# Kernel optimization log

Measured on AMD Instinct MI355X. Metric: run time of the kernel, lower is better.

The kernel has to match this reference:

```python
import jax, jax.numpy as jnp
import numpy as np

H = 128          # hidden_size
L = 3            # num_layers
N = 200_000      # total atoms across all fragments
E = 400_000      # bidirectional bonds (avg degree ~2)
G = 8192         # number of molecular subgraphs
ATOM_V = 120
BOND_V = 5


def setup_inputs() -> dict:
    key = jax.random.key(0)
    ks = jax.random.split(key, 14)
    s = 1.0 / np.sqrt(H)
    f = lambda k, shp: (jax.random.normal(k, shp, jnp.float32) * s)
    return {
        "atom_types": jax.random.randint(ks[0], (N,), 0, ATOM_V),
        "edges": jax.random.randint(ks[1], (2, E), 0, N),
        "edge_types": jax.random.randint(ks[2], (E,), 0, BOND_V),
        "node_batch": jnp.sort(jax.random.randint(ks[3], (N,), 0, G)),
        "atom_emb": f(ks[4], (ATOM_V, H)),
        "bond_emb": f(ks[5], (BOND_V, H)),
        "conv_w1": f(ks[6], (L, H, H)),
        "conv_b1": jnp.zeros((L, H), jnp.float32),
        "conv_w2": f(ks[7], (L, H, H)),
        "conv_b2": jnp.zeros((L, H), jnp.float32),
        "proj_w1": f(ks[8], (H, H)),
        "proj_b1": jnp.zeros((H,), jnp.float32),
        "proj_w2": f(ks[9], (H, H)),
        "proj_b2": jnp.zeros((H,), jnp.float32),
    }


def reference(atom_types, edges, edge_types, node_batch,
              atom_emb, bond_emb,
              conv_w1, conv_b1, conv_w2, conv_b2,
              proj_w1, proj_b1, proj_w2, proj_b2):
    # node / bond embeddings (torch clamps indices to vocab-1)
    x = atom_emb[jnp.clip(atom_types, 0, ATOM_V - 1)]       # [N, H]
    a = bond_emb[jnp.clip(edge_types, 0, BOND_V - 1)]       # [E, H]
    src, dst = edges[0], edges[1]
    # GINEConv layers: x_i' = MLP(x_i + sum_{j->i} ReLU(x_j + e_ji)), eps=0
    for l in range(L):
        m = jax.nn.relu(x[src] + a)                         # [E, H] edge messages
        agg = jax.ops.segment_sum(m, dst, num_segments=N)   # scatter-add to dst nodes
        h = x + agg
        h = jax.nn.relu(h @ conv_w1[l] + conv_b1[l])
        x = h @ conv_w2[l] + conv_b2[l]
    # per-graph mean readout
    sums = jax.ops.segment_sum(x, node_batch, num_segments=G)                      # [G, H]
    cnt = jax.ops.segment_sum(jnp.ones((N, 1), x.dtype), node_batch, num_segments=G)
    g = sums / jnp.maximum(cnt, 1.0)
    # proj: Linear -> SiLU -> Linear
    g = jax.nn.silu(g @ proj_w1 + proj_b1)
    return g @ proj_w2 + proj_b2                            # [G, H]
```

## Files before the change

kernel.cpp:

```cpp
#include <hip/hip_runtime.h>

typedef unsigned short u16;
typedef __attribute__((ext_vector_type(8))) short short8;
typedef __attribute__((ext_vector_type(4))) float f32x4;

#define HDIM 128
#define SCAN_B 512

__device__ __forceinline__ float bf2f(u16 v) {
    return __uint_as_float(((unsigned int)v) << 16);
}
__device__ __forceinline__ u16 f2bf(float f) {
    unsigned int u = __float_as_uint(f);
    unsigned int r = (u + 0x7FFFu + ((u >> 16) & 1u)) >> 16;
    return (u16)r;
}

__global__ __launch_bounds__(256) void prep_kernel(
    const float* __restrict__ w1, const float* __restrict__ w2,
    const float* __restrict__ pw1, const float* __restrict__ pw2,
    const float* __restrict__ atom_emb,
    u16* __restrict__ wt, u16* __restrict__ ebf)
{
    int gid = blockIdx.x * 256 + threadIdx.x;
    if (gid < 8 * 16384) {
        int mat = gid >> 14;
        int idx = gid & 16383;
        int n = idx >> 7, k = idx & 127;
        const float* src;
        if      (mat < 3) src = w1 + mat * 16384;
        else if (mat < 6) src = w2 + (mat - 3) * 16384;
        else if (mat == 6) src = pw1;
        else               src = pw2;
        wt[gid] = f2bf(src[k * 128 + n]);
    } else {
        int i = gid - 8 * 16384;
        if (i < 120 * 128) ebf[i] = f2bf(atom_emb[i]);
    }
}

__global__ __launch_bounds__(256) void deg_hist_kernel(
    const int* __restrict__ edges, int* __restrict__ deg, int E, int N)
{
    int e = blockIdx.x * 256 + threadIdx.x;
    if (e >= E) return;
    int d = edges[E + e];
    d = d < 0 ? 0 : (d >= N ? N - 1 : d);
    atomicAdd(&deg[d], 1);
}

__global__ __launch_bounds__(SCAN_B) void scan_block_kernel(
    const int* __restrict__ deg, int* __restrict__ offs, int* __restrict__ bsum, int N)
{
    __shared__ int tmp[SCAN_B];
    int t = threadIdx.x;
    int gid = blockIdx.x * SCAN_B + t;
    int v = (gid < N) ? deg[gid] : 0;
    tmp[t] = v;
    __syncthreads();
#pragma unroll
    for (int off = 1; off < SCAN_B; off <<= 1) {
        int add = (t >= off) ? tmp[t - off] : 0;
        __syncthreads();
        tmp[t] += add;
        __syncthreads();
    }
    if (gid < N) offs[gid] = tmp[t] - v;
    if (t == SCAN_B - 1) bsum[blockIdx.x] = tmp[t];
}

__global__ __launch_bounds__(1024) void scan_partials_kernel(int* __restrict__ bsum, int nblk)
{
    __shared__ int tmp[1024];
    int t = threadIdx.x;
    int v = (t < nblk) ? bsum[t] : 0;
    tmp[t] = v;
    __syncthreads();
#pragma unroll
    for (int off = 1; off < 1024; off <<= 1) {
        int add = (t >= off) ? tmp[t - off] : 0;
        __syncthreads();
        tmp[t] += add;
        __syncthreads();
    }
    if (t < nblk) bsum[t] = tmp[t] - v;
}

__global__ __launch_bounds__(256) void finalize_offs_kernel(
    int* __restrict__ offs, const int* __restrict__ bsum,
    int* __restrict__ cursor, int N, int E)
{
    int gid = blockIdx.x * 256 + threadIdx.x;
    if (gid < N) {
        int v = offs[gid] + bsum[gid / SCAN_B];
        offs[gid] = v;
        cursor[gid] = v;
    }
    if (gid == 0) offs[N] = E;
}

__global__ __launch_bounds__(256) void fill_csr_kernel(
    const int* __restrict__ edges, const int* __restrict__ etypes,
    int* __restrict__ cursor, int* __restrict__ csr, int E, int N)
{
    int e = blockIdx.x * 256 + threadIdx.x;
    if (e >= E) return;
    int s = edges[e], d = edges[E + e], t = etypes[e];
    s = s < 0 ? 0 : (s >= N ? N - 1 : s);
    d = d < 0 ? 0 : (d >= N ? N - 1 : d);
    t = t < 0 ? 0 : (t > 4 ? 4 : t);
    int pos = atomicAdd(&cursor[d], 1);
    csr[pos] = (s << 3) | t;
}

__global__ __launch_bounds__(512, 4) void gine_kernel(
    const u16* __restrict__ x_in, u16* __restrict__ x_out,
    const int* __restrict__ types, int use_emb, const u16* __restrict__ ebf,
    const int* __restrict__ offs, const int* __restrict__ csr,
    const float* __restrict__ bond_emb,
    const u16* __restrict__ w1t, const float* __restrict__ b1,
    const u16* __restrict__ w2t, const float* __restrict__ b2, int N)
{
    __shared__ __align__(16) u16 As[128][136];
    __shared__ __align__(16) u16 Ws[128][136];
    __shared__ __align__(16) u16 bsh[5 * 128];
    const int tid  = threadIdx.x;
    const int row0 = blockIdx.x * 128;
    const int wave = tid >> 6, lane = tid & 63;
    const int m = lane & 15, quad = lane >> 4;

    for (int i = tid; i < 640; i += 512) bsh[i] = f2bf(bond_emb[i]);
    {
        const uint4* src = (const uint4*)w1t;
        for (int i = tid; i < 2048; i += 512) {
            int n = i >> 4, k8 = i & 15;
            *(uint4*)&Ws[n][k8 * 8] = src[i];
        }
    }
    {
        const int rp = tid >> 4, c8 = (tid & 15) * 8;
        __syncthreads();
        for (int pass = 0; pass < 2; pass++) {
            int rA = (pass * 2 + 0) * 32 + rp;
            int rB = (pass * 2 + 1) * 32 + rp;
            int rowA = row0 + rA, rowB = row0 + rB;
            int rcA = rowA < N ? rowA : N - 1;
            int rcB = rowB < N ? rowB : N - 1;
            const u16 *spA, *spB;
            if (use_emb) {
                int tA = types[rcA]; tA = tA < 0 ? 0 : (tA > 119 ? 119 : tA);
                int tB = types[rcB]; tB = tB < 0 ? 0 : (tB > 119 ? 119 : tB);
                spA = ebf + (size_t)tA * 128;
                spB = ebf + (size_t)tB * 128;
            } else {
                spA = x_in + (size_t)rcA * 128;
                spB = x_in + (size_t)rcB * 128;
            }
            int jbA = offs[rcA], jeA = rowA < N ? offs[rcA + 1] : jbA;
            int jbB = offs[rcB], jeB = rowB < N ? offs[rcB + 1] : jbB;
            uint4 svA = *(const uint4*)(spA + c8);
            uint4 svB = *(const uint4*)(spB + c8);
            float accA[8], accB[8];
            {
                const u16* pA = (const u16*)&svA;
                const u16* pB = (const u16*)&svB;
#pragma unroll
                for (int i = 0; i < 8; i++) { accA[i] = bf2f(pA[i]); accB[i] = bf2f(pB[i]); }
            }
            int dA = jeA - jbA, dB = jeB - jbB;
            int dmax = dA > dB ? dA : dB;
            for (int k = 0; k < dmax; k += 2) {
                bool a0 = (k    ) < dA;
                bool a1 = (k + 1) < dA;
                bool a2 = (k    ) < dB;
                bool a3 = (k + 1) < dB;
                int v0 = a0 ? csr[jbA + k]     : 0;
                int v1 = a1 ? csr[jbA + k + 1] : 0;
                int v2 = a2 ? csr[jbB + k]     : 0;
                int v3 = a3 ? csr[jbB + k + 1] : 0;
                const u16 *g0p, *g1p, *g2p, *g3p;
                if (use_emb) {
                    int t0 = types[v0 >> 3]; t0 = t0 < 0 ? 0 : (t0 > 119 ? 119 : t0);
                    int t1 = types[v1 >> 3]; t1 = t1 < 0 ? 0 : (t1 > 119 ? 119 : t1);
                    int t2 = types[v2 >> 3]; t2 = t2 < 0 ? 0 : (t2 > 119 ? 119 : t2);
                    int t3 = types[v3 >> 3]; t3 = t3 < 0 ? 0 : (t3 > 119 ? 119 : t3);
                    g0p = ebf + (size_t)t0 * 128; g1p = ebf + (size_t)t1 * 128;
                    g2p = ebf + (size_t)t2 * 128; g3p = ebf + (size_t)t3 * 128;
                } else {
                    g0p = x_in + (size_t)(v0 >> 3) * 128;
                    g1p = x_in + (size_t)(v1 >> 3) * 128;
                    g2p = x_in + (size_t)(v2 >> 3) * 128;
                    g3p = x_in + (size_t)(v3 >> 3) * 128;
                }
                uint4 g0 = *(const uint4*)(g0p + c8);
                uint4 g1 = *(const uint4*)(g1p + c8);
                uint4 g2 = *(const uint4*)(g2p + c8);
                uint4 g3 = *(const uint4*)(g3p + c8);
                if (a0) {
                    const u16* gp = (const u16*)&g0; const u16* bp = bsh + (v0 & 7) * 128 + c8;
#pragma unroll
                    for (int i = 0; i < 8; i++) { float mm = bf2f(gp[i]) + bf2f(bp[i]); accA[i] += mm > 0.f ? mm : 0.f; }
                }
                if (a1) {
                    const u16* gp = (const u16*)&g1; const u16* bp = bsh + (v1 & 7) * 128 + c8;
#pragma unroll
                    for (int i = 0; i < 8; i++) { float mm = bf2f(gp[i]) + bf2f(bp[i]); accA[i] += mm > 0.f ? mm : 0.f; }
                }
                if (a2) {
                    const u16* gp = (const u16*)&g2; const u16* bp = bsh + (v2 & 7) * 128 + c8;
#pragma unroll
                    for (int i = 0; i < 8; i++) { float mm = bf2f(gp[i]) + bf2f(bp[i]); accB[i] += mm > 0.f ? mm : 0.f; }
                }
                if (a3) {
                    const u16* gp = (const u16*)&g3; const u16* bp = bsh + (v3 & 7) * 128 + c8;
#pragma unroll
                    for (int i = 0; i < 8; i++) { float mm = bf2f(gp[i]) + bf2f(bp[i]); accB[i] += mm > 0.f ? mm : 0.f; }
                }
            }
            uint4 ovA = make_uint4(0u, 0u, 0u, 0u), ovB = make_uint4(0u, 0u, 0u, 0u);
            if (rowA < N) {
                u16* op = (u16*)&ovA;
#pragma unroll
                for (int i = 0; i < 8; i++) op[i] = f2bf(accA[i]);
            }
            if (rowB < N) {
                u16* op = (u16*)&ovB;
#pragma unroll
                for (int i = 0; i < 8; i++) op[i] = f2bf(accB[i]);
            }
            *(uint4*)&As[rA][c8] = ovA;
            *(uint4*)&As[rB][c8] = ovB;
        }
    }
    __syncthreads();

    f32x4 acc[8];
#pragma unroll
    for (int c = 0; c < 8; c++) acc[c] = (f32x4){0.f, 0.f, 0.f, 0.f};
#pragma unroll
    for (int q = 0; q < 4; q++) {
        short8 a = *(const short8*)&As[wave * 16 + m][q * 32 + quad * 8];
#pragma unroll
        for (int c = 0; c < 8; c++) {
            short8 b = *(const short8*)&Ws[c * 16 + m][q * 32 + quad * 8];
            acc[c] = __builtin_amdgcn_mfma_f32_16x16x32_bf16(a, b, acc[c], 0, 0, 0);
        }
    }
    __syncthreads();
    {
        const uint4* src = (const uint4*)w2t;
        for (int i = tid; i < 2048; i += 512) {
            int n = i >> 4, k8 = i & 15;
            *(uint4*)&Ws[n][k8 * 8] = src[i];
        }
    }
#pragma unroll
    for (int c = 0; c < 8; c++) {
        int col = c * 16 + m;
        float bias = b1[col];
#pragma unroll
        for (int r = 0; r < 4; r++) {
            float v = acc[c][r] + bias;
            v = v > 0.f ? v : 0.f;
            As[wave * 16 + quad * 4 + r][col] = f2bf(v);
        }
    }
    __syncthreads();
    f32x4 acc2[8];
#pragma unroll
    for (int c = 0; c < 8; c++) acc2[c] = (f32x4){0.f, 0.f, 0.f, 0.f};
#pragma unroll
    for (int q = 0; q < 4; q++) {
        short8 a = *(const short8*)&As[wave * 16 + m][q * 32 + quad * 8];
#pragma unroll
        for (int c = 0; c < 8; c++) {
            short8 b = *(const short8*)&Ws[c * 16 + m][q * 32 + quad * 8];
            acc2[c] = __builtin_amdgcn_mfma_f32_16x16x32_bf16(a, b, acc2[c], 0, 0, 0);
        }
    }
    __syncthreads();
#pragma unroll
    for (int c = 0; c < 8; c++) {
        int col = c * 16 + m;
        float bias = b2[col];
#pragma unroll
        for (int r = 0; r < 4; r++)
            As[wave * 16 + quad * 4 + r][col] = f2bf(acc2[c][r] + bias);
    }
    __syncthreads();
    for (int i = tid; i < 2048; i += 512) {
        int r = i >> 4, c8 = (i & 15) * 8;
        int row = row0 + r;
        if (row < N) *(uint4*)(x_out + (size_t)row * 128 + c8) = *(const uint4*)&As[r][c8];
    }
}

__global__ __launch_bounds__(256) void readout_mean_kernel(
    const u16* __restrict__ x, const int* __restrict__ nb,
    u16* __restrict__ gm, int N)
{
    __shared__ int range[2];
    __shared__ float part[16][128];
    int b = blockIdx.x;
    int tid = threadIdx.x;
    if (tid < 2) {
        int target = b + tid;
        int lo = 0, hi = N;
        while (lo < hi) {
            int mid = (lo + hi) >> 1;
            if (nb[mid] < target) lo = mid + 1; else hi = mid;
        }
        range[tid] = lo;
    }
    __syncthreads();
    int s = range[0], e = range[1];
    int rg = tid >> 4, c8 = (tid & 15) * 8;
    float acc[8];
#pragma unroll
    for (int i = 0; i < 8; i++) acc[i] = 0.f;
    for (int n = s + rg; n < e; n += 16) {
        uint4 v = *(const uint4*)(x + (size_t)n * 128 + c8);
        const u16* vp = (const u16*)&v;
#pragma unroll
        for (int i = 0; i < 8; i++) acc[i] += bf2f(vp[i]);
    }
#pragma unroll
    for (int i = 0; i < 8; i++) part[rg][c8 + i] = acc[i];
    __syncthreads();
    if (tid < 128) {
        float sum = 0.f;
#pragma unroll
        for (int g = 0; g < 16; g++) sum += part[g][tid];
        float cnt = (float)((e - s) > 0 ? (e - s) : 1);
        gm[(size_t)b * 128 + tid] = f2bf(sum / cnt);
    }
}

__global__ __launch_bounds__(256) void proj_kernel(
    const u16* __restrict__ gm, float* __restrict__ out,
    const u16* __restrict__ pw1t, const float* __restrict__ pb1,
    const u16* __restrict__ pw2t, const float* __restrict__ pb2, int G)
{
    __shared__ __align__(16) u16 As[64][136];
    __shared__ __align__(16) u16 Ws[128][136];
    const int tid  = threadIdx.x;
    const int row0 = blockIdx.x * 64;
    const int wave = tid >> 6, lane = tid & 63;
    const int m = lane & 15, quad = lane >> 4;

    {
        const uint4* src = (const uint4*)pw1t;
        for (int i = tid; i < 2048; i += 256) {
            int n = i >> 4, k8 = i & 15;
            *(uint4*)&Ws[n][k8 * 8] = src[i];
        }
    }
    for (int i = tid; i < 1024; i += 256) {
        int r = i >> 4, c8 = (i & 15) * 8;
        int row = row0 + r;
        uint4 ov = make_uint4(0u, 0u, 0u, 0u);
        if (row < G) ov = *(const uint4*)(gm + (size_t)row * 128 + c8);
        *(uint4*)&As[r][c8] = ov;
    }
    __syncthreads();
    f32x4 acc[8];
#pragma unroll
    for (int c = 0; c < 8; c++) acc[c] = (f32x4){0.f, 0.f, 0.f, 0.f};
#pragma unroll
    for (int q = 0; q < 4; q++) {
        short8 a = *(const short8*)&As[wave * 16 + m][q * 32 + quad * 8];
#pragma unroll
        for (int c = 0; c < 8; c++) {
            short8 b = *(const short8*)&Ws[c * 16 + m][q * 32 + quad * 8];
            acc[c] = __builtin_amdgcn_mfma_f32_16x16x32_bf16(a, b, acc[c], 0, 0, 0);
        }
    }
    __syncthreads();
    {
        const uint4* src = (const uint4*)pw2t;
        for (int i = tid; i < 2048; i += 256) {
            int n = i >> 4, k8 = i & 15;
            *(uint4*)&Ws[n][k8 * 8] = src[i];
        }
    }
#pragma unroll
    for (int c = 0; c < 8; c++) {
        int col = c * 16 + m;
        float bias = pb1[col];
#pragma unroll
        for (int r = 0; r < 4; r++) {
            float v = acc[c][r] + bias;
            v = v / (1.f + __expf(-v));
            As[wave * 16 + quad * 4 + r][col] = f2bf(v);
        }
    }
    __syncthreads();
    f32x4 acc2[8];
#pragma unroll
    for (int c = 0; c < 8; c++) acc2[c] = (f32x4){0.f, 0.f, 0.f, 0.f};
#pragma unroll
    for (int q = 0; q < 4; q++) {
        short8 a = *(const short8*)&As[wave * 16 + m][q * 32 + quad * 8];
#pragma unroll
        for (int c = 0; c < 8; c++) {
            short8 b = *(const short8*)&Ws[c * 16 + m][q * 32 + quad * 8];
            acc2[c] = __builtin_amdgcn_mfma_f32_16x16x32_bf16(a, b, acc2[c], 0, 0, 0);
        }
    }
#pragma unroll
    for (int c = 0; c < 8; c++) {
        int col = c * 16 + m;
        float bias = pb2[col];
#pragma unroll
        for (int r = 0; r < 4; r++) {
            int row = row0 + quad * 4 + r + wave * 16;
            if (row < G) out[(size_t)row * 128 + col] = acc2[c][r] + bias;
        }
    }
}

extern "C" void kernel_launch(void* const* d_in, const int* in_sizes, int n_in,
                              void* d_out, int out_size, void* d_ws, size_t ws_size,
                              hipStream_t stream) {
    const int*   atom_types  = (const int*)d_in[0];
    const int*   edges       = (const int*)d_in[1];
    const int*   edge_types  = (const int*)d_in[2];
    const int*   node_batch  = (const int*)d_in[3];
    const float* atom_emb    = (const float*)d_in[4];
    const float* bond_emb    = (const float*)d_in[5];
    const float* conv_w1     = (const float*)d_in[6];
    const float* conv_b1     = (const float*)d_in[7];
    const float* conv_w2     = (const float*)d_in[8];
    const float* conv_b2     = (const float*)d_in[9];
    const float* pw1         = (const float*)d_in[10];
    const float* pb1         = (const float*)d_in[11];
    const float* pw2         = (const float*)d_in[12];
    const float* pb2         = (const float*)d_in[13];
    float* out = (float*)d_out;

    const int N = in_sizes[0];
    const int E = in_sizes[2];
    const int G = out_size / HDIM;
    const int nblk = (N + SCAN_B - 1) / SCAN_B;

    size_t xA_bytes  = (size_t)N * HDIM * sizeof(u16);
    size_t xB_bytes  = (size_t)N * HDIM * sizeof(u16);
    size_t wt_bytes  = (size_t)8 * HDIM * HDIM * sizeof(u16);
    size_t ebf_bytes = (size_t)120 * HDIM * sizeof(u16);
    size_t gm_bytes  = (size_t)G * HDIM * sizeof(u16);
    size_t deg_bytes = (size_t)N * 4;
    size_t off_bytes = (size_t)(N + 1) * 4;
    size_t cur_bytes = (size_t)N * 4;
    size_t bs_bytes  = 1024 * 4;
    size_t csr_bytes = (size_t)E * 4;
    size_t need = xA_bytes + xB_bytes + wt_bytes + ebf_bytes + gm_bytes +
                  deg_bytes + off_bytes + cur_bytes + bs_bytes + csr_bytes;
    if (ws_size < need) {
        hipMemsetAsync(d_out, 0, (size_t)out_size * sizeof(float), stream);
        return;
    }
    char* p = (char*)d_ws;
    u16* xA   = (u16*)p;  p += xA_bytes;
    u16* xB   = (u16*)p;  p += xB_bytes;
    u16* wt   = (u16*)p;  p += wt_bytes;
    u16* ebf  = (u16*)p;  p += ebf_bytes;
    u16* gm   = (u16*)p;  p += gm_bytes;
    int* deg  = (int*)p;  p += deg_bytes;
    int* offs = (int*)p;  p += off_bytes;
    int* cur  = (int*)p;  p += cur_bytes;
    int* bsum = (int*)p;  p += bs_bytes;
    int* csr  = (int*)p;

    prep_kernel<<<(8 * 16384 + 120 * 128 + 255) / 256, 256, 0, stream>>>(
        conv_w1, conv_w2, pw1, pw2, atom_emb, wt, ebf);

    hipMemsetAsync(deg, 0, deg_bytes, stream);
    deg_hist_kernel<<<(E + 255) / 256, 256, 0, stream>>>(edges, deg, E, N);
    scan_block_kernel<<<nblk, SCAN_B, 0, stream>>>(deg, offs, bsum, N);
    scan_partials_kernel<<<1, 1024, 0, stream>>>(bsum, nblk);
    finalize_offs_kernel<<<(N + 255) / 256, 256, 0, stream>>>(offs, bsum, cur, N, E);
    fill_csr_kernel<<<(E + 255) / 256, 256, 0, stream>>>(edges, edge_types, cur, csr, E, N);

    const int gblocks = (N + 127) / 128;
    gine_kernel<<<gblocks, 512, 0, stream>>>(
        xB , xA, atom_types, 1, ebf, offs, csr, bond_emb,
        wt + 0 * 16384, conv_b1 + 0, wt + 3 * 16384, conv_b2 + 0, N);
    gine_kernel<<<gblocks, 512, 0, stream>>>(
        xA, xB, atom_types, 0, ebf, offs, csr, bond_emb,
        wt + 1 * 16384, conv_b1 + 128, wt + 4 * 16384, conv_b2 + 128, N);
    gine_kernel<<<gblocks, 512, 0, stream>>>(
        xB, xA, atom_types, 0, ebf, offs, csr, bond_emb,
        wt + 2 * 16384, conv_b1 + 256, wt + 5 * 16384, conv_b2 + 256, N);

    readout_mean_kernel<<<G, 256, 0, stream>>>(xA, node_batch, gm, N);
    proj_kernel<<<(G + 63) / 64, 256, 0, stream>>>(
        gm, out, wt + 6 * 16384, pb1, wt + 7 * 16384, pb2, G);
}
```

Before: 371.4 us.

## Fuse readout into projection, drop partial scan kernel, gather four rows

Merges the per-graph mean readout into the projection kernel so pooled features stay in shared memory, and removes the separate block-partial scan by having each finalize block reduce its own prefix. The gine gather loop now handles four destination rows per thread at once to raise memory-level parallelism. The fused readout runs with far fewer blocks and walks 64 graphs serially with barriers per graph, which may reduce parallelism in that phase.

```diff
diff --git a/kernel.cpp b/kernel.cpp
--- a/kernel.cpp
+++ b/kernel.cpp
@@ -69,30 +69,26 @@
     if (t == SCAN_B - 1) bsum[blockIdx.x] = tmp[t];
 }
 
-__global__ __launch_bounds__(1024) void scan_partials_kernel(int* __restrict__ bsum, int nblk)
-{
-    __shared__ int tmp[1024];
-    int t = threadIdx.x;
-    int v = (t < nblk) ? bsum[t] : 0;
-    tmp[t] = v;
-    __syncthreads();
-#pragma unroll
-    for (int off = 1; off < 1024; off <<= 1) {
-        int add = (t >= off) ? tmp[t - off] : 0;
-        __syncthreads();
-        tmp[t] += add;
-        __syncthreads();
-    }
-    if (t < nblk) bsum[t] = tmp[t] - v;
-}
-
 __global__ __launch_bounds__(256) void finalize_offs_kernel(
     int* __restrict__ offs, const int* __restrict__ bsum,
     int* __restrict__ cursor, int N, int E)
 {
-    int gid = blockIdx.x * 256 + threadIdx.x;
+    __shared__ int red[256];
+    const int tid = threadIdx.x;
+    const int B = blockIdx.x >> 1;
+    int sum = 0;
+    for (int t = tid; t < B; t += 256) sum += bsum[t];
+    red[tid] = sum;
+    __syncthreads();
+#pragma unroll
+    for (int off = 128; off > 0; off >>= 1) {
+        if (tid < off) red[tid] += red[tid + off];
+        __syncthreads();
+    }
+    int prefix = red[0];
+    int gid = blockIdx.x * 256 + tid;
     if (gid < N) {
-        int v = offs[gid] + bsum[gid / SCAN_B];
+        int v = offs[gid] + prefix;
         offs[gid] = v;
         cursor[gid] = v;
     }
@@ -140,97 +136,126 @@
     {
         const int rp = tid >> 4, c8 = (tid & 15) * 8;
         __syncthreads();
-        for (int pass = 0; pass < 2; pass++) {
-            int rA = (pass * 2 + 0) * 32 + rp;
-            int rB = (pass * 2 + 1) * 32 + rp;
-            int rowA = row0 + rA, rowB = row0 + rB;
-            int rcA = rowA < N ? rowA : N - 1;
-            int rcB = rowB < N ? rowB : N - 1;
-            const u16 *spA, *spB;
+
+        int rowA = row0 + rp,      rowB = row0 + 32 + rp;
+        int rowC = row0 + 64 + rp, rowD = row0 + 96 + rp;
+        int rcA = rowA < N ? rowA : N - 1;
+        int rcB = rowB < N ? rowB : N - 1;
+        int rcC = rowC < N ? rowC : N - 1;
+        int rcD = rowD < N ? rowD : N - 1;
+        const u16 *spA, *spB, *spC, *spD;
+        if (use_emb) {
+            int tA = types[rcA]; tA = tA < 0 ? 0 : (tA > 119 ? 119 : tA);
+            int tB = types[rcB]; tB = tB < 0 ? 0 : (tB > 119 ? 119 : tB);
+            int tC = types[rcC]; tC = tC < 0 ? 0 : (tC > 119 ? 119 : tC);
+            int tD = types[rcD]; tD = tD < 0 ? 0 : (tD > 119 ? 119 : tD);
+            spA = ebf + (size_t)tA * 128; spB = ebf + (size_t)tB * 128;
+            spC = ebf + (size_t)tC * 128; spD = ebf + (size_t)tD * 128;
+        } else {
+            spA = x_in + (size_t)rcA * 128; spB = x_in + (size_t)rcB * 128;
+            spC = x_in + (size_t)rcC * 128; spD = x_in + (size_t)rcD * 128;
+        }
+        int jbA = offs[rcA], jeA = rowA < N ? offs[rcA + 1] : jbA;
+        int jbB = offs[rcB], jeB = rowB < N ? offs[rcB + 1] : jbB;
+        int jbC = offs[rcC], jeC = rowC < N ? offs[rcC + 1] : jbC;
+        int jbD = offs[rcD], jeD = rowD < N ? offs[rcD + 1] : jbD;
+        uint4 svA = *(const uint4*)(spA + c8);
+        uint4 svB = *(const uint4*)(spB + c8);
+        uint4 svC = *(const uint4*)(spC + c8);
+        uint4 svD = *(const uint4*)(spD + c8);
+        float accA[8], accB[8], accC[8], accD[8];
+        {
+            const u16* pA = (const u16*)&svA; const u16* pB = (const u16*)&svB;
+            const u16* pC = (const u16*)&svC; const u16* pD = (const u16*)&svD;
+#pragma unroll
+            for (int i = 0; i < 8; i++) {
+                accA[i] = bf2f(pA[i]); accB[i] = bf2f(pB[i]);
+                accC[i] = bf2f(pC[i]); accD[i] = bf2f(pD[i]);
+            }
+        }
+        int dA = jeA - jbA, dB = jeB - jbB, dC = jeC - jbC, dD = jeD - jbD;
+        int dmax = dA > dB ? dA : dB;
+        dmax = dC > dmax ? dC : dmax;
+        dmax = dD > dmax ? dD : dmax;
+        for (int k = 0; k < dmax; k += 2) {
+            bool a0 = k < dA,     a1 = (k + 1) < dA;
+            bool a2 = k < dB,     a3 = (k + 1) < dB;
+            bool a4 = k < dC,     a5 = (k + 1) < dC;
+            bool a6 = k < dD,     a7 = (k + 1) < dD;
+            int v0 = a0 ? csr[jbA + k] : 0;  int v1 = a1 ? csr[jbA + k + 1] : 0;
+            int v2 = a2 ? csr[jbB + k] : 0;  int v3 = a3 ? csr[jbB + k + 1] : 0;
+            int v4 = a4 ? csr[jbC + k] : 0;  int v5 = a5 ? csr[jbC + k + 1] : 0;
+            int v6 = a6 ? csr[jbD + k] : 0;  int v7 = a7 ? csr[jbD + k + 1] : 0;
+            const u16 *p0, *p1, *p2, *p3, *p4, *p5, *p6, *p7;
             if (use_emb) {
-                int tA = types[rcA]; tA = tA < 0 ? 0 : (tA > 119 ? 119 : tA);
-                int tB = types[rcB]; tB = tB < 0 ? 0 : (tB > 119 ? 119 : tB);
-                spA = ebf + (size_t)tA * 128;
-                spB = ebf + (size_t)tB * 128;
+                int t0 = types[v0 >> 3]; t0 = t0 < 0 ? 0 : (t0 > 119 ? 119 : t0);
+                int t1 = types[v1 >> 3]; t1 = t1 < 0 ? 0 : (t1 > 119 ? 119 : t1);
+                int t2 = types[v2 >> 3]; t2 = t2 < 0 ? 0 : (t2 > 119 ? 119 : t2);
+                int t3 = types[v3 >> 3]; t3 = t3 < 0 ? 0 : (t3 > 119 ? 119 : t3);
+                int t4 = types[v4 >> 3]; t4 = t4 < 0 ? 0 : (t4 > 119 ? 119 : t4);
+                int t5 = types[v5 >> 3]; t5 = t5 < 0 ? 0 : (t5 > 119 ? 119 : t5);
+                int t6 = types[v6 >> 3]; t6 = t6 < 0 ? 0 : (t6 > 119 ? 119 : t6);
+                int t7 = types[v7 >> 3]; t7 = t7 < 0 ? 0 : (t7 > 119 ? 119 : t7);
+                p0 = ebf + (size_t)t0 * 128; p1 = ebf + (size_t)t1 * 128;
+                p2 = ebf + (size_t)t2 * 128; p3 = ebf + (size_t)t3 * 128;
+                p4 = ebf + (size_t)t4 * 128; p5 = ebf + (size_t)t5 * 128;
+                p6 = ebf + (size_t)t6 * 128; p7 = ebf + (size_t)t7 * 128;
             } else {
-                spA = x_in + (size_t)rcA * 128;
-                spB = x_in + (size_t)rcB * 128;
+                p0 = x_in + (size_t)(v0 >> 3) * 128; p1 = x_in + (size_t)(v1 >> 3) * 128;
+                p2 = x_in + (size_t)(v2 >> 3) * 128; p3 = x_in + (size_t)(v3 >> 3) * 128;
+                p4 = x_in + (size_t)(v4 >> 3) * 128; p5 = x_in + (size_t)(v5 >> 3) * 128;
+                p6 = x_in + (size_t)(v6 >> 3) * 128; p7 = x_in + (size_t)(v7 >> 3) * 128;
             }
-            int jbA = offs[rcA], jeA = rowA < N ? offs[rcA + 1] : jbA;
-            int jbB = offs[rcB], jeB = rowB < N ? offs[rcB + 1] : jbB;
-            uint4 svA = *(const uint4*)(spA + c8);
-            uint4 svB = *(const uint4*)(spB + c8);
-            float accA[8], accB[8];
-            {
-                const u16* pA = (const u16*)&svA;
-                const u16* pB = (const u16*)&svB;
-#pragma unroll
-                for (int i = 0; i < 8; i++) { accA[i] = bf2f(pA[i]); accB[i] = bf2f(pB[i]); }
-            }
-            int dA = jeA - jbA, dB = jeB - jbB;
-            int dmax = dA > dB ? dA : dB;
-            for (int k = 0; k < dmax; k += 2) {
-                bool a0 = (k    ) < dA;
-                bool a1 = (k + 1) < dA;
-                bool a2 = (k    ) < dB;
-                bool a3 = (k + 1) < dB;
-                int v0 = a0 ? csr[jbA + k]     : 0;
-                int v1 = a1 ? csr[jbA + k + 1] : 0;
-                int v2 = a2 ? csr[jbB + k]     : 0;
-                int v3 = a3 ? csr[jbB + k + 1] : 0;
-                const u16 *g0p, *g1p, *g2p, *g3p;
-                if (use_emb) {
-                    int t0 = types[v0 >> 3]; t0 = t0 < 0 ? 0 : (t0 > 119 ? 119 : t0);
-                    int t1 = types[v1 >> 3]; t1 = t1 < 0 ? 0 : (t1 > 119 ? 119 : t1);
-                    int t2 = types[v2 >> 3]; t2 = t2 < 0 ? 0 : (t2 > 119 ? 119 : t2);
-                    int t3 = types[v3 >> 3]; t3 = t3 < 0 ? 0 : (t3 > 119 ? 119 : t3);
-                    g0p = ebf + (size_t)t0 * 128; g1p = ebf + (size_t)t1 * 128;
-                    g2p = ebf + (size_t)t2 * 128; g3p = ebf + (size_t)t3 * 128;
-                } else {
-                    g0p = x_in + (size_t)(v0 >> 3) * 128;
-                    g1p = x_in + (size_t)(v1 >> 3) * 128;
-                    g2p = x_in + (size_t)(v2 >> 3) * 128;
-                    g3p = x_in + (size_t)(v3 >> 3) * 128;
-                }
-                uint4 g0 = *(const uint4*)(g0p + c8);
-                uint4 g1 = *(const uint4*)(g1p + c8);
-                uint4 g2 = *(const uint4*)(g2p + c8);
-                uint4 g3 = *(const uint4*)(g3p + c8);
-                if (a0) {
-                    const u16* gp = (const u16*)&g0; const u16* bp = bsh + (v0 & 7) * 128 + c8;
-#pragma unroll
-                    for (int i = 0; i < 8; i++) { float mm = bf2f(gp[i]) + bf2f(bp[i]); accA[i] += mm > 0.f ? mm : 0.f; }
-                }
-                if (a1) {
-                    const u16* gp = (const u16*)&g1; const u16* bp = bsh + (v1 & 7) * 128 + c8;
-#pragma unroll
-                    for (int i = 0; i < 8; i++) { float mm = bf2f(gp[i]) + bf2f(bp[i]); accA[i] += mm > 0.f ? mm : 0.f; }
-                }
-                if (a2) {
-                    const u16* gp = (const u16*)&g2; const u16* bp = bsh + (v2 & 7) * 128 + c8;
-#pragma unroll
-                    for (int i = 0; i < 8; i++) { float mm = bf2f(gp[i]) + bf2f(bp[i]); accB[i] += mm > 0.f ? mm : 0.f; }
-                }
-                if (a3) {
-                    const u16* gp = (const u16*)&g3; const u16* bp = bsh + (v3 & 7) * 128 + c8;
-#pragma unroll
-                    for (int i = 0; i < 8; i++) { float mm = bf2f(gp[i]) + bf2f(bp[i]); accB[i] += mm > 0.f ? mm : 0.f; }
-                }
-            }
-            uint4 ovA = make_uint4(0u, 0u, 0u, 0u), ovB = make_uint4(0u, 0u, 0u, 0u);
-            if (rowA < N) {
-                u16* op = (u16*)&ovA;
-#pragma unroll
-                for (int i = 0; i < 8; i++) op[i] = f2bf(accA[i]);
-            }
-            if (rowB < N) {
-                u16* op = (u16*)&ovB;
-#pragma unroll
-                for (int i = 0; i < 8; i++) op[i] = f2bf(accB[i]);
-            }
-            *(uint4*)&As[rA][c8] = ovA;
-            *(uint4*)&As[rB][c8] = ovB;
-        }
+            uint4 g0 = *(const uint4*)(p0 + c8);
+            uint4 g1 = *(const uint4*)(p1 + c8);
+            uint4 g2 = *(const uint4*)(p2 + c8);
+            uint4 g3 = *(const uint4*)(p3 + c8);
+            uint4 g4 = *(const uint4*)(p4 + c8);
+            uint4 g5 = *(const uint4*)(p5 + c8);
+            uint4 g6 = *(const uint4*)(p6 + c8);
+            uint4 g7 = *(const uint4*)(p7 + c8);
+            if (a0) { const u16* gp = (const u16*)&g0; const u16* bp = bsh + (v0 & 7) * 128 + c8;
+#pragma unroll
+                for (int i = 0; i < 8; i++) { float mm = bf2f(gp[i]) + bf2f(bp[i]); accA[i] += mm > 0.f ? mm : 0.f; } }
+            if (a1) { const u16* gp = (const u16*)&g1; const u16* bp = bsh + (v1 & 7) * 128 + c8;
+#pragma unroll
+                for (int i = 0; i < 8; i++) { float mm = bf2f(gp[i]) + bf2f(bp[i]); accA[i] += mm > 0.f ? mm : 0.f; } }
+            if (a2) { const u16* gp = (const u16*)&g2; const u16* bp = bsh + (v2 & 7) * 128 + c8;
+#pragma unroll
+                for (int i = 0; i < 8; i++) { float mm = bf2f(gp[i]) + bf2f(bp[i]); accB[i] += mm > 0.f ? mm : 0.f; } }
+            if (a3) { const u16* gp = (const u16*)&g3; const u16* bp = bsh + (v3 & 7) * 128 + c8;
+#pragma unroll
+                for (int i = 0; i < 8; i++) { float mm = bf2f(gp[i]) + bf2f(bp[i]); accB[i] += mm > 0.f ? mm : 0.f; } }
+            if (a4) { const u16* gp = (const u16*)&g4; const u16* bp = bsh + (v4 & 7) * 128 + c8;
+#pragma unroll
+                for (int i = 0; i < 8; i++) { float mm = bf2f(gp[i]) + bf2f(bp[i]); accC[i] += mm > 0.f ? mm : 0.f; } }
+            if (a5) { const u16* gp = (const u16*)&g5; const u16* bp = bsh + (v5 & 7) * 128 + c8;
+#pragma unroll
+                for (int i = 0; i < 8; i++) { float mm = bf2f(gp[i]) + bf2f(bp[i]); accC[i] += mm > 0.f ? mm : 0.f; } }
+            if (a6) { const u16* gp = (const u16*)&g6; const u16* bp = bsh + (v6 & 7) * 128 + c8;
+#pragma unroll
+                for (int i = 0; i < 8; i++) { float mm = bf2f(gp[i]) + bf2f(bp[i]); accD[i] += mm > 0.f ? mm : 0.f; } }
+            if (a7) { const u16* gp = (const u16*)&g7; const u16* bp = bsh + (v7 & 7) * 128 + c8;
+#pragma unroll
+                for (int i = 0; i < 8; i++) { float mm = bf2f(gp[i]) + bf2f(bp[i]); accD[i] += mm > 0.f ? mm : 0.f; } }
+        }
+        uint4 ovA = make_uint4(0u,0u,0u,0u), ovB = ovA, ovC = ovA, ovD = ovA;
+        if (rowA < N) { u16* op = (u16*)&ovA;
+#pragma unroll
+            for (int i = 0; i < 8; i++) op[i] = f2bf(accA[i]); }
+        if (rowB < N) { u16* op = (u16*)&ovB;
+#pragma unroll
+            for (int i = 0; i < 8; i++) op[i] = f2bf(accB[i]); }
+        if (rowC < N) { u16* op = (u16*)&ovC;
+#pragma unroll
+            for (int i = 0; i < 8; i++) op[i] = f2bf(accC[i]); }
+        if (rowD < N) { u16* op = (u16*)&ovD;
+#pragma unroll
+            for (int i = 0; i < 8; i++) op[i] = f2bf(accD[i]); }
+        *(uint4*)&As[rp][c8]      = ovA;
+        *(uint4*)&As[32 + rp][c8] = ovB;
+        *(uint4*)&As[64 + rp][c8] = ovC;
+        *(uint4*)&As[96 + rp][c8] = ovD;
     }
     __syncthreads();
 
@@ -295,56 +320,18 @@
     }
 }
 
-__global__ __launch_bounds__(256) void readout_mean_kernel(
+__global__ __launch_bounds__(256) void readout_proj_kernel(
     const u16* __restrict__ x, const int* __restrict__ nb,
-    u16* __restrict__ gm, int N)
-{
-    __shared__ int range[2];
-    __shared__ float part[16][128];
-    int b = blockIdx.x;
-    int tid = threadIdx.x;
-    if (tid < 2) {
-        int target = b + tid;
-        int lo = 0, hi = N;
-        while (lo < hi) {
-            int mid = (lo + hi) >> 1;
-            if (nb[mid] < target) lo = mid + 1; else hi = mid;
-        }
-        range[tid] = lo;
-    }
-    __syncthreads();
-    int s = range[0], e = range[1];
-    int rg = tid >> 4, c8 = (tid & 15) * 8;
-    float acc[8];
-#pragma unroll
-    for (int i = 0; i < 8; i++) acc[i] = 0.f;
-    for (int n = s + rg; n < e; n += 16) {
-        uint4 v = *(const uint4*)(x + (size_t)n * 128 + c8);
-        const u16* vp = (const u16*)&v;
-#pragma unroll
-        for (int i = 0; i < 8; i++) acc[i] += bf2f(vp[i]);
-    }
-#pragma unroll
-    for (int i = 0; i < 8; i++) part[rg][c8 + i] = acc[i];
-    __syncthreads();
-    if (tid < 128) {
-        float sum = 0.f;
-#pragma unroll
-        for (int g = 0; g < 16; g++) sum += part[g][tid];
-        float cnt = (float)((e - s) > 0 ? (e - s) : 1);
-        gm[(size_t)b * 128 + tid] = f2bf(sum / cnt);
-    }
-}
-
-__global__ __launch_bounds__(256) void proj_kernel(
-    const u16* __restrict__ gm, float* __restrict__ out,
     const u16* __restrict__ pw1t, const float* __restrict__ pb1,
-    const u16* __restrict__ pw2t, const float* __restrict__ pb2, int G)
+    const u16* __restrict__ pw2t, const float* __restrict__ pb2,
+    float* __restrict__ out, int N, int G)
 {
     __shared__ __align__(16) u16 As[64][136];
     __shared__ __align__(16) u16 Ws[128][136];
+    __shared__ float part[16][128];
+    __shared__ int bounds[65];
     const int tid  = threadIdx.x;
-    const int row0 = blockIdx.x * 64;
+    const int g0   = blockIdx.x * 64;
     const int wave = tid >> 6, lane = tid & 63;
     const int m = lane & 15, quad = lane >> 4;
 
@@ -355,14 +342,42 @@
             *(uint4*)&Ws[n][k8 * 8] = src[i];
         }
     }
-    for (int i = tid; i < 1024; i += 256) {
-        int r = i >> 4, c8 = (i & 15) * 8;
-        int row = row0 + r;
-        uint4 ov = make_uint4(0u, 0u, 0u, 0u);
-        if (row < G) ov = *(const uint4*)(gm + (size_t)row * 128 + c8);
-        *(uint4*)&As[r][c8] = ov;
-    }
-    __syncthreads();
+    if (tid < 65) {
+        int target = g0 + tid;
+        int lo = 0, hi = N;
+        while (lo < hi) {
+            int mid = (lo + hi) >> 1;
+            if (nb[mid] < target) lo = mid + 1; else hi = mid;
+        }
+        bounds[tid] = lo;
+    }
+    __syncthreads();
+
+    const int rp = tid >> 4, c8 = (tid & 15) * 8;
+    for (int i = 0; i < 64; i++) {
+        int s = bounds[i], e = bounds[i + 1];
+        float acc[8];
+#pragma unroll
+        for (int j = 0; j < 8; j++) acc[j] = 0.f;
+        for (int n = s + rp; n < e; n += 16) {
+            uint4 v = *(const uint4*)(x + (size_t)n * 128 + c8);
+            const u16* vp = (const u16*)&v;
+#pragma unroll
+            for (int j = 0; j < 8; j++) acc[j] += bf2f(vp[j]);
+        }
+#pragma unroll
+        for (int j = 0; j < 8; j++) part[rp][c8 + j] = acc[j];
+        __syncthreads();
+        if (tid < 128) {
+            float sum = 0.f;
+#pragma unroll
+            for (int g = 0; g < 16; g++) sum += part[g][tid];
+            float cnt = (float)((e - s) > 0 ? (e - s) : 1);
+            As[i][tid] = f2bf(sum / cnt);
+        }
+        __syncthreads();
+    }
+
     f32x4 acc[8];
 #pragma unroll
     for (int c = 0; c < 8; c++) acc[c] = (f32x4){0.f, 0.f, 0.f, 0.f};
@@ -413,7 +428,7 @@
         float bias = pb2[col];
 #pragma unroll
         for (int r = 0; r < 4; r++) {
-            int row = row0 + quad * 4 + r + wave * 16;
+            int row = g0 + wave * 16 + quad * 4 + r;
             if (row < G) out[(size_t)row * 128 + col] = acc2[c][r] + bias;
         }
     }
@@ -447,13 +462,12 @@
     size_t xB_bytes  = (size_t)N * HDIM * sizeof(u16);
     size_t wt_bytes  = (size_t)8 * HDIM * HDIM * sizeof(u16);
     size_t ebf_bytes = (size_t)120 * HDIM * sizeof(u16);
-    size_t gm_bytes  = (size_t)G * HDIM * sizeof(u16);
     size_t deg_bytes = (size_t)N * 4;
     size_t off_bytes = (size_t)(N + 1) * 4;
     size_t cur_bytes = (size_t)N * 4;
-    size_t bs_bytes  = 1024 * 4;
+    size_t bs_bytes  = (size_t)nblk * 4;
     size_t csr_bytes = (size_t)E * 4;
-    size_t need = xA_bytes + xB_bytes + wt_bytes + ebf_bytes + gm_bytes +
+    size_t need = xA_bytes + xB_bytes + wt_bytes + ebf_bytes +
                   deg_bytes + off_bytes + cur_bytes + bs_bytes + csr_bytes;
     if (ws_size < need) {
         hipMemsetAsync(d_out, 0, (size_t)out_size * sizeof(float), stream);
@@ -464,7 +478,6 @@
     u16* xB   = (u16*)p;  p += xB_bytes;
     u16* wt   = (u16*)p;  p += wt_bytes;
     u16* ebf  = (u16*)p;  p += ebf_bytes;
-    u16* gm   = (u16*)p;  p += gm_bytes;
     int* deg  = (int*)p;  p += deg_bytes;
     int* offs = (int*)p;  p += off_bytes;
     int* cur  = (int*)p;  p += cur_bytes;
@@ -477,7 +490,6 @@
     hipMemsetAsync(deg, 0, deg_bytes, stream);
     deg_hist_kernel<<<(E + 255) / 256, 256, 0, stream>>>(edges, deg, E, N);
     scan_block_kernel<<<nblk, SCAN_B, 0, stream>>>(deg, offs, bsum, N);
-    scan_partials_kernel<<<1, 1024, 0, stream>>>(bsum, nblk);
     finalize_offs_kernel<<<(N + 255) / 256, 256, 0, stream>>>(offs, bsum, cur, N, E);
     fill_csr_kernel<<<(E + 255) / 256, 256, 0, stream>>>(edges, edge_types, cur, csr, E, N);
 
@@ -492,7 +504,6 @@
         xB, xA, atom_types, 0, ebf, offs, csr, bond_emb,
         wt + 2 * 16384, conv_b1 + 256, wt + 5 * 16384, conv_b2 + 256, N);
 
-    readout_mean_kernel<<<G, 256, 0, stream>>>(xA, node_batch, gm, N);
-    proj_kernel<<<(G + 63) / 64, 256, 0, stream>>>(
-        gm, out, wt + 6 * 16384, pb1, wt + 7 * 16384, pb2, G);
-}
+    readout_proj_kernel<<<(G + 63) / 64, 256, 0, stream>>>(
+        xA, node_batch, wt + 6 * 16384, pb1, wt + 7 * 16384, pb2, out, N, G);
+}
```

Measured after the change: 394.9 us. +6.3%, slower.
